# Kernel tuning notes

Measured on AMD Instinct MI355X. Metric: run time of the kernel, lower is better.

The kernel has to match this reference:

```python
import jax, jax.numpy as jnp
import numpy as np

BANDWIDTH = 3

def _elup1(x):
    return jnp.where(x >= 0, x + 1.0, jnp.exp(x))

def setup_inputs() -> dict:
    key = jax.random.key(0)
    ks = jax.random.split(key, 12)
    B, T, lod, act_dim, K, H = 256, 256, 64, 32, 15, 60
    lsd = 2 * lod
    latent_obs = jax.random.normal(ks[0], (B, T, lod), jnp.float32)
    obs_vars = jax.random.uniform(ks[1], (B, T, lod), jnp.float32) * 0.1 + 0.01
    actions = jax.random.normal(ks[2], (B, T, act_dim), jnp.float32)
    initial_mean = jax.random.normal(ks[3], (B, lsd), jnp.float32)
    # initial covariance factors: cu = cl = 10 (config initial_state_covar), cs = 0
    initial_cov = jnp.stack([10.0 * jnp.ones((B, lod), jnp.float32),
                             10.0 * jnp.ones((B, lod), jnp.float32),
                             jnp.zeros((B, lod), jnp.float32)], 0)
    coeff_w = jax.random.normal(ks[4], (lsd, K), jnp.float32) * 0.05
    coeff_b = jnp.zeros((K,), jnp.float32)
    ctrl_w1 = jax.random.normal(ks[5], (act_dim, H), jnp.float32) * (1.0 / np.sqrt(act_dim))
    ctrl_b1 = jnp.zeros((H,), jnp.float32)
    ctrl_w2 = jax.random.normal(ks[6], (H, lsd), jnp.float32) * (1.0 / np.sqrt(H))
    ctrl_b2 = jnp.zeros((lsd,), jnp.float32)
    tm_basis = jax.random.normal(ks[7], (4, K, lod, lod), jnp.float32) * 0.05
    tcov_u = jnp.full((lod,), np.log(np.e ** 0.1 - 0.0), jnp.float32) * 0.0 - 2.0  # elup1(-2)~0.135
    tcov_l = jnp.zeros((lod,), jnp.float32) - 2.0
    obs_valid = jax.random.bernoulli(ks[8], 0.9, (B, T))
    return {"latent_obs": latent_obs, "obs_vars": obs_vars, "actions": actions,
            "initial_mean": initial_mean, "initial_cov": initial_cov,
            "coeff_w": coeff_w, "coeff_b": coeff_b,
            "ctrl_w1": ctrl_w1, "ctrl_b1": ctrl_b1, "ctrl_w2": ctrl_w2, "ctrl_b2": ctrl_b2,
            "tm_basis": tm_basis, "tcov_u": tcov_u, "tcov_l": tcov_l,
            "obs_valid": obs_valid}

def reference(latent_obs, obs_vars, actions, initial_mean, initial_cov,
              coeff_w, coeff_b, ctrl_w1, ctrl_b1, ctrl_w2, ctrl_b2,
              tm_basis, tcov_u, tcov_l, obs_valid):
    B, T, lod = latent_obs.shape
    idx = jnp.arange(lod)
    band = (jnp.abs(idx[:, None] - idx[None, :]) <= BANDWIDTH).astype(latent_obs.dtype)
    eye = jnp.eye(lod, dtype=latent_obs.dtype)
    tm_b = tm_basis * band  # (4, K, lod, lod), banded basis matrices
    tcu = _elup1(tcov_u)
    tcl = _elup1(tcov_l)

    def dadat(A, d):   # diag(A diag(d) A^T)
        return jnp.einsum('bij,bj->bi', A * A, d)

    def dadbt(A, d, Bm):  # diag(A diag(d) B^T)
        return jnp.einsum('bij,bj->bi', A * Bm, d)

    def step(carry, xs):
        pm, cu, cl, cs = carry
        act, obs, ov, valid = xs
        # --- observation update (factorized Kalman gain) ---
        denom = cu + ov
        qu = cu / denom
        ql = cs / denom
        res = obs - pm[:, :lod]
        post_mean_upd = pm + jnp.concatenate([qu * res, ql * res], -1)
        covf = 1.0 - qu
        pcu_u, pcl_u, pcs_u = covf * cu, cl - ql * cs, covf * cs
        v = valid[:, None]
        post_mean = jnp.where(v, post_mean_upd, pm)
        pcu = jnp.where(v, pcu_u, cu)
        pcl = jnp.where(v, pcl_u, cl)
        pcs = jnp.where(v, pcs_u, cs)
        # --- action-conditional locally-linear prediction ---
        coeff = jax.nn.softmax(post_mean @ coeff_w + coeff_b, axis=-1)  # (B, K)
        tms = jnp.einsum('bk,fkij->fbij', coeff, tm_b)  # (4, B, lod, lod)
        tm11 = tms[0] + eye
        tm12 = tms[1]
        tm21 = tms[2]
        tm22 = tms[3] + eye
        mu, ml = post_mean[:, :lod], post_mean[:, lod:]
        nmu = jnp.einsum('bij,bj->bi', tm11, mu) + jnp.einsum('bij,bj->bi', tm12, ml)
        nml = jnp.einsum('bij,bj->bi', tm21, mu) + jnp.einsum('bij,bj->bi', tm22, ml)
        ctrl = jax.nn.relu(act @ ctrl_w1 + ctrl_b1) @ ctrl_w2 + ctrl_b2
        npm = jnp.concatenate([nmu, nml], -1) + ctrl
        ncu = dadat(tm11, pcu) + 2.0 * dadbt(tm11, pcs, tm12) + dadat(tm12, pcl) + tcu
        ncl = dadat(tm21, pcu) + 2.0 * dadbt(tm21, pcs, tm22) + dadat(tm22, pcl) + tcl
        ncs = (dadbt(tm21, pcu, tm11) + dadbt(tm22, pcs, tm11)
               + dadbt(tm21, pcs, tm12) + dadbt(tm22, pcl, tm12))
        carry = (npm, ncu, ncl, ncs)
        ys = (post_mean, pcu, pcl, pcs, npm, ncu, ncl, ncs)
        return carry, ys

    icu, icl, ics = initial_cov[0], initial_cov[1], initial_cov[2]
    xs = (jnp.moveaxis(actions, 1, 0), jnp.moveaxis(latent_obs, 1, 0),
          jnp.moveaxis(obs_vars, 1, 0), jnp.moveaxis(obs_valid, 1, 0))
    _, ys = jax.lax.scan(step, (initial_mean, icu, icl, ics), xs)
    # time-major -> batch-major, matching torch.stack(..., 1)
    return tuple(jnp.moveaxis(y, 0, 1) for y in ys)
```

## Files before the change

### kernel.cpp

```cpp
#include <hip/hip_runtime.h>
#include <math.h>

namespace {
constexpr int B_ = 256, T_ = 256, LOD = 64, LSD = 128, ACTD = 32, K_ = 15, H_ = 60;
constexpr int NB = 7;
constexpr int BROW = 9;

constexpr int O_W1 = 0;
constexpr int O_W2 = O_W1 + ACTD*H_;
constexpr int O_CW = O_W2 + H_*LSD;
constexpr int O_B1 = O_CW + LSD*K_;
constexpr int O_B2 = O_B1 + H_;
constexpr int O_CB = O_B2 + LSD;
constexpr int O_TCU = O_CB + 16;
constexpr int O_TCL = O_TCU + LOD;
constexpr int O_PM  = O_TCL + LOD;
constexpr int O_CU  = O_PM + LSD;
constexpr int O_CL  = O_CU + LOD;
constexpr int O_CS  = O_CL + LOD;
constexpr int O_MU  = O_CS + LOD;
constexpr int O_ML  = O_MU + 72;
constexpr int O_PCU = O_ML + 72;
constexpr int O_PCL = O_PCU + 72;
constexpr int O_PCS = O_PCL + 72;
constexpr int O_ACT = O_PCS + 72;
constexpr int O_H   = O_ACT + ACTD;
constexpr int O_CTRL= O_H + H_;
constexpr int O_PART= O_CTRL + LSD;
constexpr int O_BANDS = O_PART + K_*8;
constexpr int O_END = O_BANDS + 4*64*BROW;

constexpr long long NBT = (long long)B_*T_;
constexpr long long OO1 = NBT*LSD;
constexpr long long OO2 = OO1 + NBT*LOD;
constexpr long long OO3 = OO2 + NBT*LOD;
constexpr long long OO4 = OO3 + NBT*LOD;
constexpr long long OO5 = OO4 + NBT*LSD;
constexpr long long OO6 = OO5 + NBT*LOD;
constexpr long long OO7 = OO6 + NBT*LOD;
}

__global__ __launch_bounds__(256, 1)
void rkn_scan_kernel(const float* __restrict__ g_obs, const float* __restrict__ g_ovar,
                     const float* __restrict__ g_act, const float* __restrict__ g_im,
                     const float* __restrict__ g_icov, const float* __restrict__ g_cw,
                     const float* __restrict__ g_cb, const float* __restrict__ g_w1,
                     const float* __restrict__ g_b1, const float* __restrict__ g_w2,
                     const float* __restrict__ g_b2, const float* __restrict__ g_tmb,
                     const float* __restrict__ g_tcu, const float* __restrict__ g_tcl,
                     const int* __restrict__ g_valid, float* __restrict__ out)
{
    __shared__ float sm[O_END];
    __shared__ int svalid;

    const int t = threadIdx.x;
    const int b = blockIdx.x;
    const int lane = t & 63;
    const int f = t >> 6;
    const int i = t & 63;

    for (int idx = t; idx < ACTD*H_; idx += 256) sm[O_W1+idx] = g_w1[idx];
    for (int idx = t; idx < H_*LSD;  idx += 256) sm[O_W2+idx] = g_w2[idx];
    for (int idx = t; idx < LSD*K_;  idx += 256) sm[O_CW+idx] = g_cw[idx];
    if (t < H_)  sm[O_B1+t] = g_b1[t];
    if (t < LSD) sm[O_B2+t] = g_b2[t];
    if (t < K_)  sm[O_CB+t] = g_cb[t];
    if (t < LOD) {
        float x = g_tcu[t]; sm[O_TCU+t] = (x >= 0.f) ? x + 1.f : expf(x);
        float y = g_tcl[t]; sm[O_TCL+t] = (y >= 0.f) ? y + 1.f : expf(y);
        sm[O_CU+t] = g_icov[0*B_*LOD + b*LOD + t];
        sm[O_CL+t] = g_icov[1*B_*LOD + b*LOD + t];
        sm[O_CS+t] = g_icov[2*B_*LOD + b*LOD + t];
    }
    if (t < LSD) sm[O_PM+t] = g_im[b*LSD + t];
    for (int idx = t; idx < 5*72; idx += 256) sm[O_MU+idx] = 0.f;

    float bas[K_][NB];
    #pragma unroll
    for (int k = 0; k < K_; ++k) {
        #pragma unroll
        for (int d = 0; d < NB; ++d) {
            int j = i - 3 + d;
            bas[k][d] = (j >= 0 && j < LOD)
                ? g_tmb[(((long long)f*K_ + k)*LOD + i)*LOD + j] : 0.f;
        }
    }

    float obs0=0.f, ov0=0.f, obs1=0.f, ov1=0.f, a0=0.f, a1=0.f;
    int v0=0, v1=0;
    if (t < LOD) {
        obs0 = g_obs [((long long)b*T_+0)*LOD + t];
        ov0  = g_ovar[((long long)b*T_+0)*LOD + t];
        obs1 = g_obs [((long long)b*T_+1)*LOD + t];
        ov1  = g_ovar[((long long)b*T_+1)*LOD + t];
    }
    if (t < ACTD) {
        a0 = g_act[((long long)b*T_+0)*ACTD + t];
        a1 = g_act[((long long)b*T_+1)*ACTD + t];
        sm[O_ACT+t] = a0;
    }
    if (t == 0) {
        v0 = g_valid[b*T_ + 0];
        v1 = g_valid[b*T_ + 1];
        svalid = v0;
    }
    __syncthreads();

    #pragma unroll 1
    for (int tt = 0; tt < T_; ++tt) {
        const long long bt = (long long)b*T_ + tt;

        if (t < LOD) {
            float cuv = sm[O_CU+i], clv = sm[O_CL+i], csv = sm[O_CS+i];
            float pmu = sm[O_PM+i], pml = sm[O_PM+64+i];
            float denom = cuv + ov0;
            float qu = cuv / denom;
            float ql = csv / denom;
            float res = obs0 - pmu;
            float pu, pl, pcu, pcl, pcs;
            if (svalid) {
                pu = pmu + qu*res;  pl = pml + ql*res;
                float covf = 1.f - qu;
                pcu = covf*cuv;  pcl = clv - ql*csv;  pcs = covf*csv;
            } else {
                pu = pmu; pl = pml; pcu = cuv; pcl = clv; pcs = csv;
            }
            sm[O_MU+3+i] = pu;   sm[O_ML+3+i] = pl;
            sm[O_PCU+3+i] = pcu; sm[O_PCL+3+i] = pcl; sm[O_PCS+3+i] = pcs;
            out[bt*LSD + i]       = pu;
            out[bt*LSD + 64 + i]  = pl;
            out[OO1 + bt*LOD + i] = pcu;
            out[OO2 + bt*LOD + i] = pcl;
            out[OO3 + bt*LOD + i] = pcs;
        } else if (t < 64 + H_) {
            int j = t - 64;
            float acc = sm[O_B1+j];
            #pragma unroll
            for (int a = 0; a < ACTD; ++a) acc += sm[O_ACT+a] * sm[O_W1 + a*H_ + j];
            sm[O_H+j] = fmaxf(acc, 0.f);
        }
        __syncthreads();

        obs0 = obs1; ov0 = ov1; a0 = a1; v0 = v1;
        {
            int tn = (tt + 2 < T_) ? tt + 2 : T_ - 1;
            if (t < LOD) {
                obs1 = g_obs [((long long)b*T_+tn)*LOD + t];
                ov1  = g_ovar[((long long)b*T_+tn)*LOD + t];
            }
            if (t < ACTD) a1 = g_act[((long long)b*T_+tn)*ACTD + t];
            if (t == 0)   v1 = g_valid[b*T_ + tn];
        }
        if (t < 120) {
            int k = t >> 3, p = t & 7, j0 = p*16;
            const float* src = (p < 4) ? &sm[O_MU+3+j0] : &sm[O_ML+3+j0-64];
            float acc = 0.f;
            #pragma unroll
            for (int jj = 0; jj < 16; ++jj) acc += src[jj] * sm[O_CW + (j0+jj)*K_ + k];
            sm[O_PART + t] = acc;
        } else if (t >= 128) {
            int ii = t - 128;
            float acc = sm[O_B2+ii];
            #pragma unroll
            for (int j = 0; j < H_; ++j) acc += sm[O_H+j] * sm[O_W2 + j*LSD + ii];
            sm[O_CTRL+ii] = acc;
        }
        __syncthreads();

        float coef;
        {
            int g = lane & 15;
            float s = -3.0e38f;
            if (g < K_) {
                s = sm[O_CB+g];
                #pragma unroll
                for (int p = 0; p < 8; ++p) s += sm[O_PART + g*8 + p];
            }
            float m = s;
            #pragma unroll
            for (int off = 1; off < 16; off <<= 1) m = fmaxf(m, __shfl_xor(m, off, 16));
            float e = (g < K_) ? expf(s - m) : 0.f;
            float ssum = e;
            #pragma unroll
            for (int off = 1; off < 16; off <<= 1) ssum += __shfl_xor(ssum, off, 16);
            coef = e / ssum;
        }
        float bnd[NB];
        #pragma unroll
        for (int d = 0; d < NB; ++d) bnd[d] = 0.f;
        #pragma unroll
        for (int k = 0; k < K_; ++k) {
            float ck = __shfl(coef, k, 16);
            #pragma unroll
            for (int d = 0; d < NB; ++d) bnd[d] += ck * bas[k][d];
        }
        if (f == 0 || f == 3) bnd[3] += 1.f;
        {
            int base = O_BANDS + (f*64 + i)*BROW;
            #pragma unroll
            for (int d = 0; d < NB; ++d) sm[base + d] = bnd[d];
        }
        __syncthreads();

        {
            const float* bd = &sm[O_BANDS];
            if (f == 0) {
                float acc = sm[O_CTRL+i];
                #pragma unroll
                for (int d = 0; d < NB; ++d)
                    acc += bd[(0*64+i)*BROW+d]*sm[O_MU+i+d]
                         + bd[(1*64+i)*BROW+d]*sm[O_ML+i+d];
                sm[O_PM+i] = acc;
                out[OO4 + bt*LSD + i] = acc;
                if (t < ACTD) sm[O_ACT+t] = a0;
                if (t == 0) svalid = v0;
            } else if (f == 1) {
                float acc = sm[O_CTRL+64+i];
                float ncs = 0.f;
                #pragma unroll
                for (int d = 0; d < NB; ++d) {
                    float Ad = bd[(0*64+i)*BROW+d], Bd = bd[(1*64+i)*BROW+d];
                    float Cd = bd[(2*64+i)*BROW+d], Dd = bd[(3*64+i)*BROW+d];
                    acc += Cd*sm[O_MU+i+d] + Dd*sm[O_ML+i+d];
                    float pu = sm[O_PCU+i+d], ps = sm[O_PCS+i+d], pl = sm[O_PCL+i+d];
                    ncs += Ad*(Cd*pu + Dd*ps) + Bd*(Cd*ps + Dd*pl);
                }
                sm[O_PM+64+i] = acc;
                out[OO4 + bt*LSD + 64 + i] = acc;
                sm[O_CS+i] = ncs;
                out[OO7 + bt*LOD + i] = ncs;
            } else if (f == 2) {
                float acc = sm[O_TCU+i];
                #pragma unroll
                for (int d = 0; d < NB; ++d) {
                    float Ad = bd[(0*64+i)*BROW+d], Bd = bd[(1*64+i)*BROW+d];
                    float pu = sm[O_PCU+i+d], ps = sm[O_PCS+i+d], pl = sm[O_PCL+i+d];
                    acc += Ad*Ad*pu + 2.f*Ad*Bd*ps + Bd*Bd*pl;
                }
                sm[O_CU+i] = acc;
                out[OO5 + bt*LOD + i] = acc;
            } else {
                float acc = sm[O_TCL+i];
                #pragma unroll
                for (int d = 0; d < NB; ++d) {
                    float Cd = bd[(2*64+i)*BROW+d], Dd = bd[(3*64+i)*BROW+d];
                    float pu = sm[O_PCU+i+d], ps = sm[O_PCS+i+d], pl = sm[O_PCL+i+d];
                    acc += Cd*Cd*pu + 2.f*Cd*Dd*ps + Dd*Dd*pl;
                }
                sm[O_CL+i] = acc;
                out[OO6 + bt*LOD + i] = acc;
            }
        }
        __syncthreads();
    }
}

extern "C" void kernel_launch(void* const* d_in, const int* in_sizes, int n_in,
                              void* d_out, int out_size, void* d_ws, size_t ws_size,
                              hipStream_t stream) {
    (void)in_sizes; (void)n_in; (void)d_ws; (void)ws_size; (void)out_size;
    rkn_scan_kernel<<<B_, 256, 0, stream>>>(
        (const float*)d_in[0],  (const float*)d_in[1],  (const float*)d_in[2],
        (const float*)d_in[3],  (const float*)d_in[4],  (const float*)d_in[5],
        (const float*)d_in[6],  (const float*)d_in[7],  (const float*)d_in[8],
        (const float*)d_in[9],  (const float*)d_in[10], (const float*)d_in[11],
        (const float*)d_in[12], (const float*)d_in[13], (const int*)d_in[14],
        (float*)d_out);
}
```

Before: 779.0 us.

## Chunk control MLP over 8 steps, DPP-reduce logits, cut per-step barriers

Observations, variances and actions for 8 timesteps are staged into shared memory per chunk. The control MLP, which does not depend on the state, is computed for the whole chunk in batch off the sequential path. The coefficient logits are now computed by every wave with DPP wave reductions instead of a partial-sum pass, so each timestep needs 3 barriers instead of 4. Work is rebalanced across the four waves, and output stores are deferred by one step so they overlap with the next step. This adds shared memory and register pressure and uses fast-math exp.

```diff
diff --git a/kernel.cpp b/kernel.cpp
--- a/kernel.cpp
+++ b/kernel.cpp
@@ -2,42 +2,59 @@
 #include <math.h>
 
 namespace {
-constexpr int B_ = 256, T_ = 256, LOD = 64, LSD = 128, ACTD = 32, K_ = 15, H_ = 60;
-constexpr int NB = 7;
-constexpr int BROW = 9;
+constexpr int B_=256, T_=256;
+constexpr int NB=7;
+constexpr int CH=8;
+constexpr int NCH=T_/CH;
 
 constexpr int O_W1 = 0;
-constexpr int O_W2 = O_W1 + ACTD*H_;
-constexpr int O_CW = O_W2 + H_*LSD;
-constexpr int O_B1 = O_CW + LSD*K_;
-constexpr int O_B2 = O_B1 + H_;
-constexpr int O_CB = O_B2 + LSD;
-constexpr int O_TCU = O_CB + 16;
-constexpr int O_TCL = O_TCU + LOD;
-constexpr int O_PM  = O_TCL + LOD;
-constexpr int O_CU  = O_PM + LSD;
-constexpr int O_CL  = O_CU + LOD;
-constexpr int O_CS  = O_CL + LOD;
-constexpr int O_MU  = O_CS + LOD;
-constexpr int O_ML  = O_MU + 72;
-constexpr int O_PCU = O_ML + 72;
-constexpr int O_PCL = O_PCU + 72;
-constexpr int O_PCS = O_PCL + 72;
-constexpr int O_ACT = O_PCS + 72;
-constexpr int O_H   = O_ACT + ACTD;
-constexpr int O_CTRL= O_H + H_;
-constexpr int O_PART= O_CTRL + LSD;
-constexpr int O_BANDS = O_PART + K_*8;
-constexpr int O_END = O_BANDS + 4*64*BROW;
+constexpr int O_W2 = O_W1+32*60;
+constexpr int O_B1 = O_W2+60*128;
+constexpr int O_B2 = O_B1+64;
+constexpr int O_TCU= O_B2+128;
+constexpr int O_TCL= O_TCU+64;
+constexpr int O_PM = O_TCL+64;
+constexpr int O_CU = O_PM+128;
+constexpr int O_CL = O_CU+64;
+constexpr int O_CS = O_CL+64;
+constexpr int O_MU = O_CS+64;
+constexpr int O_ML = O_MU+72;
+constexpr int O_PCU= O_ML+72;
+constexpr int O_PCL= O_PCU+72;
+constexpr int O_PCS= O_PCL+72;
+constexpr int O_BND= O_PCS+72;
+constexpr int O_LG = O_BND+4*7*64;
+constexpr int O_OBS= O_LG+16;
+constexpr int O_OV = O_OBS+CH*64;
+constexpr int O_ACT= O_OV+CH*64;
+constexpr int O_CT = O_ACT+CH*32;
+constexpr int O_H  = O_CT+CH*128;
+constexpr int O_END= O_H+CH*60;
 
 constexpr long long NBT = (long long)B_*T_;
-constexpr long long OO1 = NBT*LSD;
-constexpr long long OO2 = OO1 + NBT*LOD;
-constexpr long long OO3 = OO2 + NBT*LOD;
-constexpr long long OO4 = OO3 + NBT*LOD;
-constexpr long long OO5 = OO4 + NBT*LSD;
-constexpr long long OO6 = OO5 + NBT*LOD;
-constexpr long long OO7 = OO6 + NBT*LOD;
+constexpr long long OO1 = NBT*128;
+constexpr long long OO2 = OO1 + NBT*64;
+constexpr long long OO3 = OO2 + NBT*64;
+constexpr long long OO4 = OO3 + NBT*64;
+constexpr long long OO5 = OO4 + NBT*128;
+constexpr long long OO6 = OO5 + NBT*64;
+constexpr long long OO7 = OO6 + NBT*64;
+}
+
+template <int CTRL>
+__device__ __forceinline__ float dpp_add(float x) {
+    int v = __builtin_amdgcn_update_dpp(0, __float_as_int(x), CTRL, 0xf, 0xf, false);
+    return x + __int_as_float(v);
+}
+__device__ __forceinline__ float wave_red64(float x) {
+    x = dpp_add<0xB1>(x);
+    x = dpp_add<0x4E>(x);
+    x = dpp_add<0x124>(x);
+    x = dpp_add<0x128>(x);
+    float a = __int_as_float(__builtin_amdgcn_readlane(__float_as_int(x), 16));
+    float b = __int_as_float(__builtin_amdgcn_readlane(__float_as_int(x), 32));
+    float c = __int_as_float(__builtin_amdgcn_readlane(__float_as_int(x), 48));
+    return x + a + b + c;
 }
 
 __global__ __launch_bounds__(256, 1)
@@ -50,208 +67,238 @@
                      const float* __restrict__ g_tcu, const float* __restrict__ g_tcl,
                      const int* __restrict__ g_valid, float* __restrict__ out)
 {
-    __shared__ float sm[O_END];
-    __shared__ int svalid;
+    __shared__ __align__(16) float sm[O_END];
+    __shared__ int s_val[CH];
 
     const int t = threadIdx.x;
     const int b = blockIdx.x;
-    const int lane = t & 63;
     const int f = t >> 6;
     const int i = t & 63;
 
-    for (int idx = t; idx < ACTD*H_; idx += 256) sm[O_W1+idx] = g_w1[idx];
-    for (int idx = t; idx < H_*LSD;  idx += 256) sm[O_W2+idx] = g_w2[idx];
-    for (int idx = t; idx < LSD*K_;  idx += 256) sm[O_CW+idx] = g_cw[idx];
-    if (t < H_)  sm[O_B1+t] = g_b1[t];
-    if (t < LSD) sm[O_B2+t] = g_b2[t];
-    if (t < K_)  sm[O_CB+t] = g_cb[t];
-    if (t < LOD) {
-        float x = g_tcu[t]; sm[O_TCU+t] = (x >= 0.f) ? x + 1.f : expf(x);
-        float y = g_tcl[t]; sm[O_TCL+t] = (y >= 0.f) ? y + 1.f : expf(y);
-        sm[O_CU+t] = g_icov[0*B_*LOD + b*LOD + t];
-        sm[O_CL+t] = g_icov[1*B_*LOD + b*LOD + t];
-        sm[O_CS+t] = g_icov[2*B_*LOD + b*LOD + t];
-    }
-    if (t < LSD) sm[O_PM+t] = g_im[b*LSD + t];
+    for (int idx = t; idx < 32*60;  idx += 256) sm[O_W1+idx] = g_w1[idx];
+    for (int idx = t; idx < 60*128; idx += 256) sm[O_W2+idx] = g_w2[idx];
+    if (t < 60)  sm[O_B1+t] = g_b1[t];
+    if (t < 128) sm[O_B2+t] = g_b2[t];
+    if (t < 64) {
+        float x = g_tcu[t]; sm[O_TCU+t] = (x >= 0.f) ? x + 1.f : __expf(x);
+        float y = g_tcl[t]; sm[O_TCL+t] = (y >= 0.f) ? y + 1.f : __expf(y);
+        sm[O_CU+t] = g_icov[0*B_*64 + b*64 + t];
+        sm[O_CL+t] = g_icov[1*B_*64 + b*64 + t];
+        sm[O_CS+t] = g_icov[2*B_*64 + b*64 + t];
+    }
+    if (t < 128) sm[O_PM+t] = g_im[b*128 + t];
     for (int idx = t; idx < 5*72; idx += 256) sm[O_MU+idx] = 0.f;
 
-    float bas[K_][NB];
+    float cwa[4], cwb[4], cbq[4];
     #pragma unroll
-    for (int k = 0; k < K_; ++k) {
+    for (int q = 0; q < 4; ++q) {
+        int k = 4*f + q;
+        bool ok = (k < 15);
+        cwa[q] = ok ? g_cw[i*15 + k]      : 0.f;
+        cwb[q] = ok ? g_cw[(64+i)*15 + k] : 0.f;
+        cbq[q] = ok ? g_cb[k] * (1.f/64.f) : 0.f;
+    }
+
+    float bas[15][NB];
+    #pragma unroll
+    for (int k = 0; k < 15; ++k) {
         #pragma unroll
         for (int d = 0; d < NB; ++d) {
             int j = i - 3 + d;
-            bas[k][d] = (j >= 0 && j < LOD)
-                ? g_tmb[(((long long)f*K_ + k)*LOD + i)*LOD + j] : 0.f;
-        }
-    }
-
-    float obs0=0.f, ov0=0.f, obs1=0.f, ov1=0.f, a0=0.f, a1=0.f;
-    int v0=0, v1=0;
-    if (t < LOD) {
-        obs0 = g_obs [((long long)b*T_+0)*LOD + t];
-        ov0  = g_ovar[((long long)b*T_+0)*LOD + t];
-        obs1 = g_obs [((long long)b*T_+1)*LOD + t];
-        ov1  = g_ovar[((long long)b*T_+1)*LOD + t];
-    }
-    if (t < ACTD) {
-        a0 = g_act[((long long)b*T_+0)*ACTD + t];
-        a1 = g_act[((long long)b*T_+1)*ACTD + t];
-        sm[O_ACT+t] = a0;
-    }
-    if (t == 0) {
-        v0 = g_valid[b*T_ + 0];
-        v1 = g_valid[b*T_ + 1];
-        svalid = v0;
-    }
-    __syncthreads();
+            bas[k][d] = (j >= 0 && j < 64)
+                ? g_tmb[(((long long)f*15 + k)*64 + i)*64 + j] : 0.f;
+        }
+    }
+
+    const float* pobs = g_obs  + (size_t)b*T_*64;
+    const float* pov  = g_ovar + (size_t)b*T_*64;
+    const float* pact = g_act  + (size_t)b*T_*32;
+    const int*   pval = g_valid + (size_t)b*T_;
+    const size_t bt0  = (size_t)b*T_;
+
+    float4 pfA = {0,0,0,0}, pfB = {0,0,0,0};
+    int vpf = 0;
+    {
+        if (t < 128)  pfA = *(const float4*)(pobs + t*4);
+        else          pfA = *(const float4*)(pov + (t-128)*4);
+        if (t < 64)   pfB = *(const float4*)(pact + t*4);
+        if (t >= 64 && t < 64+CH) vpf = pval[t-64];
+    }
+
+    float h0 = 0.f, h1 = 0.f;
 
     #pragma unroll 1
-    for (int tt = 0; tt < T_; ++tt) {
-        const long long bt = (long long)b*T_ + tt;
-
-        if (t < LOD) {
+    for (int c = 0; c < NCH; ++c) {
+        if (t < 128)  *(float4*)&sm[O_OBS + t*4] = pfA;
+        else          *(float4*)&sm[O_OV + (t-128)*4] = pfA;
+        if (t < 64)   *(float4*)&sm[O_ACT + t*4] = pfB;
+        if (t >= 64 && t < 64+CH) s_val[t-64] = vpf;
+        __syncthreads();
+
+        if (c + 1 < NCH) {
+            const int co = (c+1)*CH;
+            if (t < 128)  pfA = *(const float4*)(pobs + co*64 + t*4);
+            else          pfA = *(const float4*)(pov  + co*64 + (t-128)*4);
+            if (t < 64)   pfB = *(const float4*)(pact + co*32 + t*4);
+            if (t >= 64 && t < 64+CH) vpf = pval[co + t-64];
+        }
+
+        #pragma unroll 1
+        for (int r = 0; r < 2; ++r) {
+            int slot = t + r*256;
+            int s = slot >> 6, j = slot & 63;
+            if (j < 60) {
+                float acc = sm[O_B1+j];
+                #pragma unroll
+                for (int a = 0; a < 32; ++a)
+                    acc += sm[O_ACT + s*32 + a] * sm[O_W1 + a*60 + j];
+                sm[O_H + s*60 + j] = fmaxf(acc, 0.f);
+            }
+        }
+        __syncthreads();
+
+        #pragma unroll 1
+        for (int r = 0; r < 4; ++r) {
+            int slot = t + r*256;
+            int s = slot >> 7, ii = slot & 127;
+            float acc = sm[O_B2+ii];
+            #pragma unroll
+            for (int j = 0; j < 60; ++j)
+                acc += sm[O_H + s*60 + j] * sm[O_W2 + j*128 + ii];
+            sm[O_CT + s*128 + ii] = acc;
+        }
+        __syncthreads();
+
+        #pragma unroll 1
+        for (int s = 0; s < CH; ++s) {
+            const int tt = c*CH + s;
+            const size_t bt = bt0 + tt;
+
+            if (tt > 0) {
+                const size_t bp = bt - 1;
+                if (f == 0)      { out[OO4 + bp*128 + i] = h0; out[OO4 + bp*128 + 64 + i] = h1; }
+                else if (f == 1)   out[OO5 + bp*64 + i] = h0;
+                else if (f == 2)   out[OO7 + bp*64 + i] = h0;
+                else               out[OO6 + bp*64 + i] = h0;
+            }
+
             float cuv = sm[O_CU+i], clv = sm[O_CL+i], csv = sm[O_CS+i];
             float pmu = sm[O_PM+i], pml = sm[O_PM+64+i];
-            float denom = cuv + ov0;
-            float qu = cuv / denom;
-            float ql = csv / denom;
-            float res = obs0 - pmu;
-            float pu, pl, pcu, pcl, pcs;
-            if (svalid) {
-                pu = pmu + qu*res;  pl = pml + ql*res;
-                float covf = 1.f - qu;
-                pcu = covf*cuv;  pcl = clv - ql*csv;  pcs = covf*csv;
-            } else {
-                pu = pmu; pl = pml; pcu = cuv; pcl = clv; pcs = csv;
-            }
-            sm[O_MU+3+i] = pu;   sm[O_ML+3+i] = pl;
-            sm[O_PCU+3+i] = pcu; sm[O_PCL+3+i] = pcl; sm[O_PCS+3+i] = pcs;
-            out[bt*LSD + i]       = pu;
-            out[bt*LSD + 64 + i]  = pl;
-            out[OO1 + bt*LOD + i] = pcu;
-            out[OO2 + bt*LOD + i] = pcl;
-            out[OO3 + bt*LOD + i] = pcs;
-        } else if (t < 64 + H_) {
-            int j = t - 64;
-            float acc = sm[O_B1+j];
-            #pragma unroll
-            for (int a = 0; a < ACTD; ++a) acc += sm[O_ACT+a] * sm[O_W1 + a*H_ + j];
-            sm[O_H+j] = fmaxf(acc, 0.f);
-        }
-        __syncthreads();
-
-        obs0 = obs1; ov0 = ov1; a0 = a1; v0 = v1;
-        {
-            int tn = (tt + 2 < T_) ? tt + 2 : T_ - 1;
-            if (t < LOD) {
-                obs1 = g_obs [((long long)b*T_+tn)*LOD + t];
-                ov1  = g_ovar[((long long)b*T_+tn)*LOD + t];
-            }
-            if (t < ACTD) a1 = g_act[((long long)b*T_+tn)*ACTD + t];
-            if (t == 0)   v1 = g_valid[b*T_ + tn];
-        }
-        if (t < 120) {
-            int k = t >> 3, p = t & 7, j0 = p*16;
-            const float* src = (p < 4) ? &sm[O_MU+3+j0] : &sm[O_ML+3+j0-64];
-            float acc = 0.f;
-            #pragma unroll
-            for (int jj = 0; jj < 16; ++jj) acc += src[jj] * sm[O_CW + (j0+jj)*K_ + k];
-            sm[O_PART + t] = acc;
-        } else if (t >= 128) {
-            int ii = t - 128;
-            float acc = sm[O_B2+ii];
-            #pragma unroll
-            for (int j = 0; j < H_; ++j) acc += sm[O_H+j] * sm[O_W2 + j*LSD + ii];
-            sm[O_CTRL+ii] = acc;
-        }
-        __syncthreads();
-
-        float coef;
-        {
-            int g = lane & 15;
-            float s = -3.0e38f;
-            if (g < K_) {
-                s = sm[O_CB+g];
-                #pragma unroll
-                for (int p = 0; p < 8; ++p) s += sm[O_PART + g*8 + p];
-            }
-            float m = s;
-            #pragma unroll
-            for (int off = 1; off < 16; off <<= 1) m = fmaxf(m, __shfl_xor(m, off, 16));
-            float e = (g < K_) ? expf(s - m) : 0.f;
-            float ssum = e;
-            #pragma unroll
-            for (int off = 1; off < 16; off <<= 1) ssum += __shfl_xor(ssum, off, 16);
-            coef = e / ssum;
-        }
-        float bnd[NB];
-        #pragma unroll
-        for (int d = 0; d < NB; ++d) bnd[d] = 0.f;
-        #pragma unroll
-        for (int k = 0; k < K_; ++k) {
-            float ck = __shfl(coef, k, 16);
-            #pragma unroll
-            for (int d = 0; d < NB; ++d) bnd[d] += ck * bas[k][d];
-        }
-        if (f == 0 || f == 3) bnd[3] += 1.f;
-        {
-            int base = O_BANDS + (f*64 + i)*BROW;
-            #pragma unroll
-            for (int d = 0; d < NB; ++d) sm[base + d] = bnd[d];
-        }
-        __syncthreads();
-
-        {
-            const float* bd = &sm[O_BANDS];
+            float ob  = sm[O_OBS + s*64 + i], ovv = sm[O_OV + s*64 + i];
+            const int vld = s_val[s];
+            float inv = 1.f/(cuv + ovv);
+            float qu = cuv*inv, ql = csv*inv;
+            float res = ob - pmu;
+            float covf = 1.f - qu;
+            float pu  = vld ? pmu + qu*res : pmu;
+            float pl  = vld ? pml + ql*res : pml;
+            float pcu = vld ? covf*cuv     : cuv;
+            float pcl = vld ? clv - ql*csv : clv;
+            float pcs = vld ? covf*csv     : csv;
+
+            if (f == 0)      { sm[O_MU+3+i] = pu; sm[O_ML+3+i] = pl; }
+            else if (f == 1)   sm[O_PCU+3+i] = pcu;
+            else if (f == 2)   sm[O_PCL+3+i] = pcl;
+            else               sm[O_PCS+3+i] = pcs;
+
+            float p0 = cbq[0] + pu*cwa[0] + pl*cwb[0];
+            float p1 = cbq[1] + pu*cwa[1] + pl*cwb[1];
+            float p2 = cbq[2] + pu*cwa[2] + pl*cwb[2];
+            float p3 = cbq[3] + pu*cwa[3] + pl*cwb[3];
+            p0 = wave_red64(p0); p1 = wave_red64(p1);
+            p2 = wave_red64(p2); p3 = wave_red64(p3);
+            if (i == 0) {
+                sm[O_LG + 4*f + 0] = p0; sm[O_LG + 4*f + 1] = p1;
+                sm[O_LG + 4*f + 2] = p2; sm[O_LG + 4*f + 3] = p3;
+            }
+            __syncthreads();
+
+            if (f == 0)      { out[bt*128 + i] = pu; out[bt*128 + 64 + i] = pl; }
+            else if (f == 1)   out[OO1 + bt*64 + i] = pcu;
+            else if (f == 2)   out[OO2 + bt*64 + i] = pcl;
+            else               out[OO3 + bt*64 + i] = pcs;
+
+            float lgv[15];
+            #pragma unroll
+            for (int k = 0; k < 15; ++k) lgv[k] = sm[O_LG+k];
+            float mx = lgv[0];
+            #pragma unroll
+            for (int k = 1; k < 15; ++k) mx = fmaxf(mx, lgv[k]);
+            float ssum = 0.f;
+            #pragma unroll
+            for (int k = 0; k < 15; ++k) { lgv[k] = __expf(lgv[k]-mx); ssum += lgv[k]; }
+            float isv = 1.f/ssum;
+
+            float bnd[NB] = {0,0,0,0,0,0,0};
+            #pragma unroll
+            for (int k = 0; k < 15; ++k) {
+                #pragma unroll
+                for (int d = 0; d < NB; ++d) bnd[d] += lgv[k]*bas[k][d];
+            }
+            #pragma unroll
+            for (int d = 0; d < NB; ++d) bnd[d] *= isv;
+            if (f == 0 || f == 3) bnd[3] += 1.f;
+            #pragma unroll
+            for (int d = 0; d < NB; ++d) sm[O_BND + (f*7+d)*64 + i] = bnd[d];
+            __syncthreads();
+
             if (f == 0) {
-                float acc = sm[O_CTRL+i];
-                #pragma unroll
-                for (int d = 0; d < NB; ++d)
-                    acc += bd[(0*64+i)*BROW+d]*sm[O_MU+i+d]
-                         + bd[(1*64+i)*BROW+d]*sm[O_ML+i+d];
-                sm[O_PM+i] = acc;
-                out[OO4 + bt*LSD + i] = acc;
-                if (t < ACTD) sm[O_ACT+t] = a0;
-                if (t == 0) svalid = v0;
+                float nmu = sm[O_CT + s*128 + i];
+                float nml = sm[O_CT + s*128 + 64 + i];
+                #pragma unroll
+                for (int d = 0; d < NB; ++d) {
+                    float mu_ = sm[O_MU+i+d], ml_ = sm[O_ML+i+d];
+                    float Bv = sm[O_BND + (1*7+d)*64 + i];
+                    float Cv = sm[O_BND + (2*7+d)*64 + i];
+                    float Dv = sm[O_BND + (3*7+d)*64 + i];
+                    nmu += bnd[d]*mu_ + Bv*ml_;
+                    nml += Cv*mu_ + Dv*ml_;
+                }
+                sm[O_PM+i] = nmu; sm[O_PM+64+i] = nml;
+                h0 = nmu; h1 = nml;
             } else if (f == 1) {
-                float acc = sm[O_CTRL+64+i];
-                float ncs = 0.f;
+                float acc = sm[O_TCU+i];
                 #pragma unroll
                 for (int d = 0; d < NB; ++d) {
-                    float Ad = bd[(0*64+i)*BROW+d], Bd = bd[(1*64+i)*BROW+d];
-                    float Cd = bd[(2*64+i)*BROW+d], Dd = bd[(3*64+i)*BROW+d];
-                    acc += Cd*sm[O_MU+i+d] + Dd*sm[O_ML+i+d];
-                    float pu = sm[O_PCU+i+d], ps = sm[O_PCS+i+d], pl = sm[O_PCL+i+d];
-                    ncs += Ad*(Cd*pu + Dd*ps) + Bd*(Cd*ps + Dd*pl);
+                    float Av = sm[O_BND + (0*7+d)*64 + i];
+                    float Bv = bnd[d];
+                    float puv = sm[O_PCU+i+d], psv = sm[O_PCS+i+d], plv = sm[O_PCL+i+d];
+                    acc += Av*Av*puv + 2.f*Av*Bv*psv + Bv*Bv*plv;
                 }
-                sm[O_PM+64+i] = acc;
-                out[OO4 + bt*LSD + 64 + i] = acc;
-                sm[O_CS+i] = ncs;
-                out[OO7 + bt*LOD + i] = ncs;
+                sm[O_CU+i] = acc; h0 = acc;
             } else if (f == 2) {
-                float acc = sm[O_TCU+i];
+                float acc = 0.f;
                 #pragma unroll
                 for (int d = 0; d < NB; ++d) {
-                    float Ad = bd[(0*64+i)*BROW+d], Bd = bd[(1*64+i)*BROW+d];
-                    float pu = sm[O_PCU+i+d], ps = sm[O_PCS+i+d], pl = sm[O_PCL+i+d];
-                    acc += Ad*Ad*pu + 2.f*Ad*Bd*ps + Bd*Bd*pl;
+                    float Av = sm[O_BND + (0*7+d)*64 + i];
+                    float Bv = sm[O_BND + (1*7+d)*64 + i];
+                    float Dv = sm[O_BND + (3*7+d)*64 + i];
+                    float Cv = bnd[d];
+                    float puv = sm[O_PCU+i+d], psv = sm[O_PCS+i+d], plv = sm[O_PCL+i+d];
+                    acc += Av*(Cv*puv + Dv*psv) + Bv*(Cv*psv + Dv*plv);
                 }
-                sm[O_CU+i] = acc;
-                out[OO5 + bt*LOD + i] = acc;
+                sm[O_CS+i] = acc; h0 = acc;
             } else {
                 float acc = sm[O_TCL+i];
                 #pragma unroll
                 for (int d = 0; d < NB; ++d) {
-                    float Cd = bd[(2*64+i)*BROW+d], Dd = bd[(3*64+i)*BROW+d];
-                    float pu = sm[O_PCU+i+d], ps = sm[O_PCS+i+d], pl = sm[O_PCL+i+d];
-                    acc += Cd*Cd*pu + 2.f*Cd*Dd*ps + Dd*Dd*pl;
+                    float Cv = sm[O_BND + (2*7+d)*64 + i];
+                    float Dv = bnd[d];
+                    float puv = sm[O_PCU+i+d], psv = sm[O_PCS+i+d], plv = sm[O_PCL+i+d];
+                    acc += Cv*Cv*puv + 2.f*Cv*Dv*psv + Dv*Dv*plv;
                 }
-                sm[O_CL+i] = acc;
-                out[OO6 + bt*LOD + i] = acc;
-            }
-        }
-        __syncthreads();
+                sm[O_CL+i] = acc; h0 = acc;
+            }
+            __syncthreads();
+        }
+    }
+
+    {
+        const size_t bp = bt0 + (T_-1);
+        if (f == 0)      { out[OO4 + bp*128 + i] = h0; out[OO4 + bp*128 + 64 + i] = h1; }
+        else if (f == 1)   out[OO5 + bp*64 + i] = h0;
+        else if (f == 2)   out[OO7 + bp*64 + i] = h0;
+        else               out[OO6 + bp*64 + i] = h0;
     }
 }
 
```

New measurement: 711.3 us. -8.7%, faster.
